# Kernel tuning notes

Hardware: AMD Instinct MI355X
Metric: run time of the kernel (lower is better)

## Reference

```python
import jax, jax.numpy as jnp
import numpy as np

N_BLOCKS = 100
LAYERS_PER_BLOCK = 10
D = 100
D_OUT = 10
BATCH = 65536


def setup_inputs() -> dict:
    key = jax.random.key(0)
    ks = jax.random.split(key, 6)
    bound = 1.0 / np.sqrt(D)  # PyTorch default Linear init bound
    x = jax.random.normal(ks[0], (BATCH, D), dtype=jnp.float32)
    # Stacked weights: [n_blocks, layers_per_block, out, in]
    W = jax.random.uniform(ks[1], (N_BLOCKS, LAYERS_PER_BLOCK, D, D), jnp.float32, -bound, bound)
    b = jax.random.uniform(ks[2], (N_BLOCKS, LAYERS_PER_BLOCK, D), jnp.float32, -bound, bound)
    Wf = jax.random.uniform(ks[3], (D_OUT, D), jnp.float32, -bound, bound)
    bf = jax.random.uniform(ks[4], (D_OUT,), jnp.float32, -bound, bound)
    return {"x": x, "W": W, "b": b, "Wf": Wf, "bf": bf}


def reference(x, W, b, Wf, bf):
    def layer_step(y, wb):
        w, bb = wb  # w: [D, D] (out, in), bb: [D]
        return jax.nn.relu(y @ w.T + bb), None

    def block_step(xb, wb):
        Wb, bb = wb  # [LAYERS_PER_BLOCK, D, D], [LAYERS_PER_BLOCK, D]
        y, _ = jax.lax.scan(layer_step, xb, (Wb, bb))
        return xb + y, None

    out, _ = jax.lax.scan(block_step, x, (W, b))
    return out @ Wf.T + bf
```

## Files before the change

kernel.cpp:

```cpp
#include <hip/hip_runtime.h>
#include <hip/hip_bf16.h>

#define N_LAYERS 1000
#define DD 100
#define DOUT 10
#define TM 64
#define ROWB 264
#define PLANE (TM * ROWB)
#define SMEM_BYTES (2 * PLANE)
#define ROW32 (32 * ROWB)
#define LCHUNK 14336
#define LSTRIDE (2 * LCHUNK)

typedef short s4v __attribute__((ext_vector_type(4)));
typedef short s8v __attribute__((ext_vector_type(8)));
typedef float f16v __attribute__((ext_vector_type(16)));

__device__ __forceinline__ unsigned short f2bf(float f) {
  __hip_bfloat16 h = __float2bfloat16(f);
  return *reinterpret_cast<unsigned short*>(&h);
}
__device__ __forceinline__ float bf2f(unsigned short h) {
  return __uint_as_float(((unsigned)h) << 16);
}

__global__ __launch_bounds__(256)
void presplit_kernel(const float* __restrict__ W, const float* __restrict__ b,
                     char* __restrict__ hi_g) {
  int idx = blockIdx.x * 256 + threadIdx.x;
  if (idx >= N_LAYERS * 2 * 7 * 2 * 64) return;
  int lane = idx & 63;
  int f = (idx >> 6) & 1;
  int r = idx >> 7;
  int ks = r % 7;
  int q = r / 7;
  int g = q & 1;
  int L = q >> 1;
  int n = g * 64 + f * 32 + (lane & 31);
  int k0 = ks * 16 + (lane >> 5) * 8;
  s8v hv;
#pragma unroll
  for (int j = 0; j < 8; ++j) {
    int k = k0 + j;
    float v = 0.0f;
    if (n < DD) {
      if (k < DD) v = W[((size_t)L * DD + n) * DD + k];
      else if (k == DD) v = b[(size_t)L * DD + n];
    }
    hv[j] = (short)f2bf(v);
  }
  *(s8v*)(hi_g + (size_t)idx * 16) = hv;
}

__device__ __forceinline__ void wload_f32(s8v* h, int L, int ks, int g,
                                          int l31, int lhi,
                                          const float* __restrict__ W_g,
                                          const float* __restrict__ b_g) {
  int k0 = ks * 16 + lhi * 8;
#pragma unroll
  for (int f = 0; f < 2; ++f) {
    int n = g * 64 + f * 32 + l31;
    s8v hv;
#pragma unroll
    for (int j = 0; j < 8; ++j) {
      int k = k0 + j;
      float v = 0.0f;
      if (n < DD) {
        if (k < DD) v = W_g[((size_t)L * DD + n) * DD + k];
        else if (k == DD) v = b_g[(size_t)L * DD + n];
      }
      hv[j] = (short)f2bf(v);
    }
    h[f] = hv;
  }
}

template <int PRE>
__device__ __forceinline__ void wload(s8v* h, const char* __restrict__ pH,
                                      int off, int L, int ks, int g, int l31, int lhi,
                                      const float* __restrict__ W_g,
                                      const float* __restrict__ b_g) {
  if (PRE) {
    h[0] = *(const s8v*)(pH + off);
    h[1] = *(const s8v*)(pH + off + 1024);
  } else {
    wload_f32(h, L, ks, g, l31, lhi, W_g, b_g);
  }
}

template <int PRE>
__device__ __forceinline__ void do_layer(
    int L, const char* __restrict__ rb, char* __restrict__ wb,
    int g, int l31, int lhi,
    const char* __restrict__ pH, int woff,
    s8v (&wh)[2][2], f16v (&xr)[2][2],
    const float* __restrict__ W_g, const float* __restrict__ b_g) {
  f16v acc[2][2];
#pragma unroll
  for (int mi = 0; mi < 2; ++mi)
#pragma unroll
    for (int f = 0; f < 2; ++f)
#pragma unroll
      for (int r = 0; r < 16; ++r) acc[mi][f][r] = 0.0f;

#pragma unroll
  for (int ks = 0; ks < 7; ++ks) {
    const int s = ks & 1;
    s4v a0 = *(const s4v*)(rb + ks * 32);
    s4v a1 = *(const s4v*)(rb + ks * 32 + 8);
    s4v b0 = *(const s4v*)(rb + ROW32 + ks * 32);
    s4v b1 = *(const s4v*)(rb + ROW32 + ks * 32 + 8);
    s8v ah0 = __builtin_shufflevector(a0, a1, 0, 1, 2, 3, 4, 5, 6, 7);
    s8v ah1 = __builtin_shufflevector(b0, b1, 0, 1, 2, 3, 4, 5, 6, 7);
    acc[0][0] = __builtin_amdgcn_mfma_f32_32x32x16_bf16(wh[s][0], ah0, acc[0][0], 0, 0, 0);
    acc[0][1] = __builtin_amdgcn_mfma_f32_32x32x16_bf16(wh[s][1], ah0, acc[0][1], 0, 0, 0);
    acc[1][0] = __builtin_amdgcn_mfma_f32_32x32x16_bf16(wh[s][0], ah1, acc[1][0], 0, 0, 0);
    acc[1][1] = __builtin_amdgcn_mfma_f32_32x32x16_bf16(wh[s][1], ah1, acc[1][1], 0, 0, 0);

    if (ks < 5) {
      wload<PRE>(wh[s], pH, woff + (ks + 2) * 2048, L, ks + 2, g, l31, lhi, W_g, b_g);
    } else if (ks == 6 && L + 1 < N_LAYERS) {
      wload<PRE>(wh[0], pH, woff + LSTRIDE,        L + 1, 0, g, l31, lhi, W_g, b_g);
      wload<PRE>(wh[1], pH, woff + LSTRIDE + 2048, L + 1, 1, g, l31, lhi, W_g, b_g);
    }
  }

  const bool bend = ((L % 10) == 9);
#pragma unroll
  for (int mi = 0; mi < 2; ++mi) {
    char* dstm = wb + mi * ROW32;
#pragma unroll
    for (int f = 0; f < 2; ++f) {
#pragma unroll
      for (int q = 0; q < 4; ++q) {
        const int n0 = g * 64 + f * 32 + 8 * q + 4 * lhi;
        char* dst = dstm + f * 64 + q * 16;
        if (n0 == 100) {
          s4v hq;
          hq[0] = (short)0x3F80; hq[1] = 0; hq[2] = 0; hq[3] = 0;
          *(s4v*)dst = hq;
        } else {
          s4v hq;
#pragma unroll
          for (int j = 0; j < 4; ++j) {
            const int r = q * 4 + j;
            float o = fmaxf(acc[mi][f][r], 0.0f);
            if (bend) { o += xr[mi][f][r]; xr[mi][f][r] = o; }
            hq[j] = (short)f2bf(o);
          }
          *(s4v*)dst = hq;
        }
      }
    }
  }
  __syncthreads();
}

template <int PRE>
__global__ __launch_bounds__(128, 2)
void resnet_main(const float* __restrict__ x_g,
                 const float* __restrict__ W_g, const float* __restrict__ b_g,
                 const float* __restrict__ Wf_g, const float* __restrict__ bf_g,
                 float* __restrict__ out_g,
                 const char* __restrict__ whi_g) {
  extern __shared__ char smem[];

  const int tid = threadIdx.x;
  const int lane = tid & 63;
  const int g = tid >> 6;
  const int l31 = lane & 31;
  const int lhi = lane >> 5;
  const size_t mbase = (size_t)blockIdx.x * TM;

  for (int idx = tid; idx < TM * 16; idx += 128) {
    int m = idx >> 4, kb = idx & 15;
    s4v h0, h1;
#pragma unroll
    for (int j = 0; j < 8; ++j) {
      int k = kb * 8 + j;
      float v = (k < DD) ? x_g[(mbase + m) * DD + k] : (k == DD ? 1.0f : 0.0f);
      if (j < 4) h0[j] = (short)f2bf(v);
      else       h1[j - 4] = (short)f2bf(v);
    }
    char* p = smem + m * ROWB + kb * 16;
    *(s4v*)p = h0;
    *(s4v*)(p + 8) = h1;
  }

  f16v xr[2][2];
#pragma unroll
  for (int mi = 0; mi < 2; ++mi)
#pragma unroll
    for (int f = 0; f < 2; ++f)
#pragma unroll
      for (int r = 0; r < 16; ++r) {
        int n = g * 64 + f * 32 + (r & 3) + 8 * (r >> 2) + 4 * lhi;
        xr[mi][f][r] = (n < DD) ? x_g[(mbase + mi * 32 + l31) * DD + n] : 0.0f;
      }

  const char* pH = whi_g + g * LCHUNK + lane * 16;
  s8v wh[2][2];
  wload<PRE>(wh[0], pH, 0,    0, 0, g, l31, lhi, W_g, b_g);
  wload<PRE>(wh[1], pH, 2048, 0, 1, g, l31, lhi, W_g, b_g);

  __syncthreads();

  const char* rbA = smem + l31 * ROWB + lhi * 16;
  const char* rbB = rbA + PLANE;
  char* wbA = smem + l31 * ROWB + g * 128 + lhi * 8;
  char* wbB = wbA + PLANE;

  int woff = 0;
  for (int L = 0; L < N_LAYERS; L += 2) {
    do_layer<PRE>(L,     rbA, wbB, g, l31, lhi, pH, woff,           wh, xr, W_g, b_g);
    do_layer<PRE>(L + 1, rbB, wbA, g, l31, lhi, pH, woff + LSTRIDE, wh, xr, W_g, b_g);
    woff += 2 * LSTRIDE;
  }

  if (tid < TM) {
    int m = tid;
    const char* p = smem + m * ROWB;
    float xv[104];
#pragma unroll
    for (int kb = 0; kb < 13; ++kb) {
      s4v h0 = *(const s4v*)(p + kb * 16);
      s4v h1 = *(const s4v*)(p + kb * 16 + 8);
#pragma unroll
      for (int j = 0; j < 4; ++j) {
        xv[kb * 8 + j]     = bf2f((unsigned short)h0[j]);
        xv[kb * 8 + 4 + j] = bf2f((unsigned short)h1[j]);
      }
    }
#pragma unroll
    for (int o = 0; o < DOUT; ++o) {
      float s = bf_g[o];
#pragma unroll
      for (int k = 0; k < DD; ++k) s += xv[k] * Wf_g[o * DD + k];
      out_g[(mbase + m) * DOUT + o] = s;
    }
  }
}

extern "C" void kernel_launch(void* const* d_in, const int* in_sizes, int n_in,
                              void* d_out, int out_size, void* d_ws, size_t ws_size,
                              hipStream_t stream) {
  const float* x = (const float*)d_in[0];
  const float* W = (const float*)d_in[1];
  const float* b = (const float*)d_in[2];
  const float* Wf = (const float*)d_in[3];
  const float* bf = (const float*)d_in[4];
  float* out = (float*)d_out;

  const size_t need = (size_t)N_LAYERS * 2 * LCHUNK;
  const int nwg = 65536 / TM;
  if (ws_size >= need) {
    char* whi = (char*)d_ws;
    const int chunks = N_LAYERS * 2 * 7 * 2 * 64;
    presplit_kernel<<<(chunks + 255) / 256, 256, 0, stream>>>(W, b, whi);
    (void)hipFuncSetAttribute(reinterpret_cast<const void*>(resnet_main<1>),
                              hipFuncAttributeMaxDynamicSharedMemorySize, SMEM_BYTES);
    resnet_main<1><<<nwg, 128, SMEM_BYTES, stream>>>(x, W, b, Wf, bf, out, whi);
  } else {
    (void)hipFuncSetAttribute(reinterpret_cast<const void*>(resnet_main<0>),
                              hipFuncAttributeMaxDynamicSharedMemorySize, SMEM_BYTES);
    resnet_main<0><<<nwg, 128, SMEM_BYTES, stream>>>(x, W, b, Wf, bf, out, nullptr);
  }
}
```

Baseline: 2.270 ms.

## Split row halves across four waves per block instead of two

Each workgroup now uses four waves (256 threads). Each wave handles one 32-row half of the 64-row tile and one 64-column output group, where before two waves each covered both row halves. This halves the per-wave accumulator and residual register footprint and doubles the waves per tile, with launch bounds raised to (256,4) to raise occupancy and latency hiding. In exchange, each weight fragment is now loaded by two waves, doubling weight load traffic per block, and each layer barrier now synchronizes four waves.

```diff
diff --git a/kernel.cpp b/kernel.cpp
--- a/kernel.cpp
+++ b/kernel.cpp
@@ -76,80 +76,70 @@
 }
 
 template <int PRE>
-__device__ __forceinline__ void wload(s8v* h, const char* __restrict__ pH,
-                                      int off, int L, int ks, int g, int l31, int lhi,
-                                      const float* __restrict__ W_g,
-                                      const float* __restrict__ b_g) {
-  if (PRE) {
-    h[0] = *(const s8v*)(pH + off);
-    h[1] = *(const s8v*)(pH + off + 1024);
-  } else {
-    wload_f32(h, L, ks, g, l31, lhi, W_g, b_g);
-  }
-}
-
-template <int PRE>
 __device__ __forceinline__ void do_layer(
     int L, const char* __restrict__ rb, char* __restrict__ wb,
     int g, int l31, int lhi,
     const char* __restrict__ pH, int woff,
-    s8v (&wh)[2][2], f16v (&xr)[2][2],
+    s8v (&wh)[2][2], f16v (&xr)[2],
     const float* __restrict__ W_g, const float* __restrict__ b_g) {
-  f16v acc[2][2];
-#pragma unroll
-  for (int mi = 0; mi < 2; ++mi)
-#pragma unroll
-    for (int f = 0; f < 2; ++f)
-#pragma unroll
-      for (int r = 0; r < 16; ++r) acc[mi][f][r] = 0.0f;
+  f16v acc[2];
+#pragma unroll
+  for (int f = 0; f < 2; ++f)
+#pragma unroll
+    for (int r = 0; r < 16; ++r) acc[f][r] = 0.0f;
 
 #pragma unroll
   for (int ks = 0; ks < 7; ++ks) {
     const int s = ks & 1;
     s4v a0 = *(const s4v*)(rb + ks * 32);
     s4v a1 = *(const s4v*)(rb + ks * 32 + 8);
-    s4v b0 = *(const s4v*)(rb + ROW32 + ks * 32);
-    s4v b1 = *(const s4v*)(rb + ROW32 + ks * 32 + 8);
-    s8v ah0 = __builtin_shufflevector(a0, a1, 0, 1, 2, 3, 4, 5, 6, 7);
-    s8v ah1 = __builtin_shufflevector(b0, b1, 0, 1, 2, 3, 4, 5, 6, 7);
-    acc[0][0] = __builtin_amdgcn_mfma_f32_32x32x16_bf16(wh[s][0], ah0, acc[0][0], 0, 0, 0);
-    acc[0][1] = __builtin_amdgcn_mfma_f32_32x32x16_bf16(wh[s][1], ah0, acc[0][1], 0, 0, 0);
-    acc[1][0] = __builtin_amdgcn_mfma_f32_32x32x16_bf16(wh[s][0], ah1, acc[1][0], 0, 0, 0);
-    acc[1][1] = __builtin_amdgcn_mfma_f32_32x32x16_bf16(wh[s][1], ah1, acc[1][1], 0, 0, 0);
+    s8v ah = __builtin_shufflevector(a0, a1, 0, 1, 2, 3, 4, 5, 6, 7);
+    acc[0] = __builtin_amdgcn_mfma_f32_32x32x16_bf16(wh[s][0], ah, acc[0], 0, 0, 0);
+    acc[1] = __builtin_amdgcn_mfma_f32_32x32x16_bf16(wh[s][1], ah, acc[1], 0, 0, 0);
 
     if (ks < 5) {
-      wload<PRE>(wh[s], pH, woff + (ks + 2) * 2048, L, ks + 2, g, l31, lhi, W_g, b_g);
+      if (PRE) {
+        const char* p = pH + woff + (ks + 2) * 2048;
+        wh[s][0] = *(const s8v*)(p);
+        wh[s][1] = *(const s8v*)(p + 1024);
+      } else {
+        wload_f32(wh[s], L, ks + 2, g, l31, lhi, W_g, b_g);
+      }
     } else if (ks == 6 && L + 1 < N_LAYERS) {
-      wload<PRE>(wh[0], pH, woff + LSTRIDE,        L + 1, 0, g, l31, lhi, W_g, b_g);
-      wload<PRE>(wh[1], pH, woff + LSTRIDE + 2048, L + 1, 1, g, l31, lhi, W_g, b_g);
+      if (PRE) {
+        const char* p = pH + woff + LSTRIDE;
+        wh[0][0] = *(const s8v*)(p);
+        wh[0][1] = *(const s8v*)(p + 1024);
+        wh[1][0] = *(const s8v*)(p + 2048);
+        wh[1][1] = *(const s8v*)(p + 3072);
+      } else {
+        wload_f32(wh[0], L + 1, 0, g, l31, lhi, W_g, b_g);
+        wload_f32(wh[1], L + 1, 1, g, l31, lhi, W_g, b_g);
+      }
     }
   }
 
   const bool bend = ((L % 10) == 9);
 #pragma unroll
-  for (int mi = 0; mi < 2; ++mi) {
-    char* dstm = wb + mi * ROW32;
-#pragma unroll
-    for (int f = 0; f < 2; ++f) {
-#pragma unroll
-      for (int q = 0; q < 4; ++q) {
-        const int n0 = g * 64 + f * 32 + 8 * q + 4 * lhi;
-        char* dst = dstm + f * 64 + q * 16;
-        if (n0 == 100) {
-          s4v hq;
-          hq[0] = (short)0x3F80; hq[1] = 0; hq[2] = 0; hq[3] = 0;
-          *(s4v*)dst = hq;
-        } else {
-          s4v hq;
-#pragma unroll
-          for (int j = 0; j < 4; ++j) {
-            const int r = q * 4 + j;
-            float o = fmaxf(acc[mi][f][r], 0.0f);
-            if (bend) { o += xr[mi][f][r]; xr[mi][f][r] = o; }
-            hq[j] = (short)f2bf(o);
-          }
-          *(s4v*)dst = hq;
+  for (int f = 0; f < 2; ++f) {
+#pragma unroll
+    for (int q = 0; q < 4; ++q) {
+      const int n0 = g * 64 + f * 32 + 8 * q + 4 * lhi;
+      char* dst = wb + f * 64 + q * 16;
+      if (n0 == 100) {
+        s4v hq;
+        hq[0] = (short)0x3F80; hq[1] = 0; hq[2] = 0; hq[3] = 0;
+        *(s4v*)dst = hq;
+      } else {
+        s4v hq;
+#pragma unroll
+        for (int j = 0; j < 4; ++j) {
+          const int r = q * 4 + j;
+          float o = fmaxf(acc[f][r], 0.0f);
+          if (bend) { o += xr[f][r]; xr[f][r] = o; }
+          hq[j] = (short)f2bf(o);
         }
+        *(s4v*)dst = hq;
       }
     }
   }
@@ -157,7 +147,7 @@
 }
 
 template <int PRE>
-__global__ __launch_bounds__(128, 2)
+__global__ __launch_bounds__(256, 4)
 void resnet_main(const float* __restrict__ x_g,
                  const float* __restrict__ W_g, const float* __restrict__ b_g,
                  const float* __restrict__ Wf_g, const float* __restrict__ bf_g,
@@ -167,12 +157,14 @@
 
   const int tid = threadIdx.x;
   const int lane = tid & 63;
-  const int g = tid >> 6;
+  const int wv = tid >> 6;
+  const int mi = wv & 1;
+  const int g = wv >> 1;
   const int l31 = lane & 31;
   const int lhi = lane >> 5;
   const size_t mbase = (size_t)blockIdx.x * TM;
 
-  for (int idx = tid; idx < TM * 16; idx += 128) {
+  for (int idx = tid; idx < TM * 16; idx += 256) {
     int m = idx >> 4, kb = idx & 15;
     s4v h0, h1;
 #pragma unroll
@@ -187,27 +179,32 @@
     *(s4v*)(p + 8) = h1;
   }
 
-  f16v xr[2][2];
-#pragma unroll
-  for (int mi = 0; mi < 2; ++mi)
-#pragma unroll
-    for (int f = 0; f < 2; ++f)
-#pragma unroll
-      for (int r = 0; r < 16; ++r) {
-        int n = g * 64 + f * 32 + (r & 3) + 8 * (r >> 2) + 4 * lhi;
-        xr[mi][f][r] = (n < DD) ? x_g[(mbase + mi * 32 + l31) * DD + n] : 0.0f;
-      }
-
-  const char* pH = whi_g + g * LCHUNK + lane * 16;
+  f16v xr[2];
+#pragma unroll
+  for (int f = 0; f < 2; ++f)
+#pragma unroll
+    for (int r = 0; r < 16; ++r) {
+      int n = g * 64 + f * 32 + (r & 3) + 8 * (r >> 2) + 4 * lhi;
+      xr[f][r] = (n < DD) ? x_g[(mbase + mi * 32 + l31) * DD + n] : 0.0f;
+    }
+
+  const char* pH = whi_g + (size_t)g * LCHUNK + lane * 16;
   s8v wh[2][2];
-  wload<PRE>(wh[0], pH, 0,    0, 0, g, l31, lhi, W_g, b_g);
-  wload<PRE>(wh[1], pH, 2048, 0, 1, g, l31, lhi, W_g, b_g);
+  if (PRE) {
+    wh[0][0] = *(const s8v*)(pH);
+    wh[0][1] = *(const s8v*)(pH + 1024);
+    wh[1][0] = *(const s8v*)(pH + 2048);
+    wh[1][1] = *(const s8v*)(pH + 3072);
+  } else {
+    wload_f32(wh[0], 0, 0, g, l31, lhi, W_g, b_g);
+    wload_f32(wh[1], 0, 1, g, l31, lhi, W_g, b_g);
+  }
 
   __syncthreads();
 
-  const char* rbA = smem + l31 * ROWB + lhi * 16;
+  const char* rbA = smem + l31 * ROWB + mi * ROW32 + lhi * 16;
   const char* rbB = rbA + PLANE;
-  char* wbA = smem + l31 * ROWB + g * 128 + lhi * 8;
+  char* wbA = smem + l31 * ROWB + mi * ROW32 + g * 128 + lhi * 8;
   char* wbB = wbA + PLANE;
 
   int woff = 0;
@@ -259,10 +256,10 @@
     presplit_kernel<<<(chunks + 255) / 256, 256, 0, stream>>>(W, b, whi);
     (void)hipFuncSetAttribute(reinterpret_cast<const void*>(resnet_main<1>),
                               hipFuncAttributeMaxDynamicSharedMemorySize, SMEM_BYTES);
-    resnet_main<1><<<nwg, 128, SMEM_BYTES, stream>>>(x, W, b, Wf, bf, out, whi);
+    resnet_main<1><<<nwg, 256, SMEM_BYTES, stream>>>(x, W, b, Wf, bf, out, whi);
   } else {
     (void)hipFuncSetAttribute(reinterpret_cast<const void*>(resnet_main<0>),
                               hipFuncAttributeMaxDynamicSharedMemorySize, SMEM_BYTES);
-    resnet_main<0><<<nwg, 128, SMEM_BYTES, stream>>>(x, W, b, Wf, bf, out, nullptr);
-  }
-}
+    resnet_main<0><<<nwg, 256, SMEM_BYTES, stream>>>(x, W, b, Wf, bf, out, nullptr);
+  }
+}
```

Result: slower. 2.405 ms (+6.0%).
